# Optimization experiments

Measured on AMD Instinct MI355X. Metric: run time of the kernel, lower is better.

## Reference

```python
import jax, jax.numpy as jnp
import numpy as np

S, D, H, F = 4096, 1024, 16, 4096
DH = D // H  # 64
EPS = 1e-6


def _layer_norm(x, scale, bias):
    mu = jnp.mean(x, axis=-1, keepdims=True)
    var = jnp.mean(jnp.square(x - mu), axis=-1, keepdims=True)
    return (x - mu) * jax.lax.rsqrt(var + EPS) * scale + bias


def setup_inputs() -> dict:
    key = jax.random.key(0)
    ks = jax.random.split(key, 12)
    s = 0.02
    return {
        "x": jax.random.normal(ks[0], (S, D), jnp.float32),
        "Wq": jax.random.normal(ks[1], (D, H, DH), jnp.float32) * s,
        "bq": jnp.zeros((H, DH), jnp.float32),
        "Wk": jax.random.normal(ks[2], (D, H, DH), jnp.float32) * s,
        "bk": jnp.zeros((H, DH), jnp.float32),
        "Wv": jax.random.normal(ks[3], (D, H, DH), jnp.float32) * s,
        "bv": jnp.zeros((H, DH), jnp.float32),
        "Wo": jax.random.normal(ks[4], (H, DH, D), jnp.float32) * s,
        "bo": jnp.zeros((D,), jnp.float32),
        "ln1_scale": jnp.ones((D,), jnp.float32),
        "ln1_bias": jnp.zeros((D,), jnp.float32),
        "ln2_scale": jnp.ones((D,), jnp.float32),
        "ln2_bias": jnp.zeros((D,), jnp.float32),
        "W1": jax.random.normal(ks[5], (D, F), jnp.float32) * s,
        "b1": jnp.zeros((F,), jnp.float32),
        "W2": jax.random.normal(ks[6], (F, D), jnp.float32) * s,
        "b2": jnp.zeros((D,), jnp.float32),
    }


def reference(x, Wq, bq, Wk, bk, Wv, bv, Wo, bo,
              ln1_scale, ln1_bias, ln2_scale, ln2_bias,
              W1, b1, W2, b2):
    # --- attention block (pre-LN, no mask, no dropout, no RoPE) ---
    y = _layer_norm(x, ln1_scale, ln1_bias)            # [S, D]
    q = jnp.einsum("sd,dhk->shk", y, Wq) + bq          # [S, H, DH]
    k = jnp.einsum("sd,dhk->shk", y, Wk) + bk
    v = jnp.einsum("sd,dhk->shk", y, Wv) + bv
    scale = jnp.float32(1.0 / np.sqrt(DH))
    scores = jnp.einsum("qhd,khd->hqk", q * scale, k)  # [H, S, S]
    w = jax.nn.softmax(scores, axis=-1)
    ctx = jnp.einsum("hqk,khd->qhd", w, v)             # [S, H, DH]
    attn_out = jnp.einsum("qhd,hdo->qo", ctx, Wo) + bo  # [S, D]
    x = x + attn_out
    # --- FFN block ---
    y = _layer_norm(x, ln2_scale, ln2_bias)
    y = jax.nn.gelu(y @ W1 + b1, approximate=False)
    y = y @ W2 + b2
    return x + y
```

## Files before the change

kernel.cpp:

```cpp
#include <hip/hip_runtime.h>
#include <cstdint>
#include <cstddef>


typedef __attribute__((ext_vector_type(8))) __bf16 bf16x8;
typedef __attribute__((ext_vector_type(4))) float f32x4;
typedef __attribute__((ext_vector_type(2))) float f32x2;
typedef __attribute__((ext_vector_type(16))) float f32x16;
typedef __attribute__((ext_vector_type(4))) unsigned int u32x4;

__device__ inline unsigned short f2bf(float f) {
  unsigned int u = __float_as_uint(f);
  u += 0x7fffu + ((u >> 16) & 1u);
  return (unsigned short)(u >> 16);
}

__device__ inline void gload_lds16(const unsigned short* g, unsigned short* l) {
  __builtin_amdgcn_global_load_lds(
      (const __attribute__((address_space(1))) void*)g,
      (__attribute__((address_space(3))) void*)l, 16, 0, 0);
}

__global__ __launch_bounds__(256) void prep_all(
    const float* __restrict__ Wq, const float* __restrict__ Wk,
    const float* __restrict__ Wv, const float* __restrict__ Wo,
    const float* __restrict__ W1, const float* __restrict__ W2,
    const float* __restrict__ bq, const float* __restrict__ bk,
    const float* __restrict__ bv,
    unsigned short* __restrict__ WqkvT, unsigned short* __restrict__ WoT,
    unsigned short* __restrict__ W1T, unsigned short* __restrict__ W2T,
    float* __restrict__ bqkv) {
  int b = blockIdx.x;
  if (b < 12) {
    int i = b * 256 + threadIdx.x;
    bqkv[i] = (i < 1024) ? bq[i] : (i < 2048 ? bk[i - 1024] : bv[i - 2048]);
    return;
  }
  b -= 12;
  const float* in;
  unsigned short* out;
  int K, N, nbx;
  if (b < 4096) {
    const int sel = b >> 10;
    in = (sel == 0) ? Wq : (sel == 1) ? Wk : (sel == 2) ? Wv : Wo;
    out = (sel == 3) ? WoT : WqkvT + (size_t)sel * 1024 * 1024;
    K = 1024; N = 1024; nbx = 32; b &= 1023;
  } else if (b < 8192) {
    b -= 4096; in = W1; out = W1T; K = 1024; N = 4096; nbx = 128;
  } else {
    b -= 8192; in = W2; out = W2T; K = 4096; N = 1024; nbx = 32;
  }
  const int nb = (b % nbx) * 32, kb = (b / nbx) * 32;
  __shared__ float t[32][33];
  const int tx = threadIdx.x & 31, ty = threadIdx.x >> 5;
#pragma unroll
  for (int i = 0; i < 32; i += 8)
    t[ty + i][tx] = in[(size_t)(kb + ty + i) * N + nb + tx];
  __syncthreads();
#pragma unroll
  for (int i = 0; i < 32; i += 8)
    out[(size_t)(nb + ty + i) * K + kb + tx] = f2bf(t[tx][ty + i]);
}

__global__ __launch_bounds__(256) void ln_kernel(const float* __restrict__ x,
                                                 const float* __restrict__ gamma,
                                                 const float* __restrict__ beta,
                                                 unsigned short* __restrict__ y) {
  int row = blockIdx.x, tid = threadIdx.x;
  const float4 v = ((const float4*)(x + (size_t)row * 1024))[tid];
  float s = v.x + v.y + v.z + v.w;
#pragma unroll
  for (int off = 1; off < 64; off <<= 1) s += __shfl_xor(s, off);
  __shared__ float red1[4], red2[4];
  int wave = tid >> 6;
  if ((tid & 63) == 0) red1[wave] = s;
  __syncthreads();
  float mu = (red1[0] + red1[1] + red1[2] + red1[3]) * (1.0f / 1024.0f);
  float dx = v.x - mu, dy = v.y - mu, dz = v.z - mu, dw = v.w - mu;
  float s2 = dx * dx + dy * dy + dz * dz + dw * dw;
#pragma unroll
  for (int off = 1; off < 64; off <<= 1) s2 += __shfl_xor(s2, off);
  if ((tid & 63) == 0) red2[wave] = s2;
  __syncthreads();
  float var = (red2[0] + red2[1] + red2[2] + red2[3]) * (1.0f / 1024.0f);
  float inv = rsqrtf(var + 1e-6f);
  int c = tid * 4;
  ushort4 o;
  o.x = f2bf(dx * inv * gamma[c + 0] + beta[c + 0]);
  o.y = f2bf(dy * inv * gamma[c + 1] + beta[c + 1]);
  o.z = f2bf(dz * inv * gamma[c + 2] + beta[c + 2]);
  o.w = f2bf(dw * inv * gamma[c + 3] + beta[c + 3]);
  ((ushort4*)(y + (size_t)row * 1024))[tid] = o;
}

template <bool GELU, bool RES, bool OUTBF, bool SCALEQ>
__global__ __launch_bounds__(512, 2) void gemm8(
    const unsigned short* __restrict__ A,
    const unsigned short* __restrict__ BT,
    const float* __restrict__ bias,
    const float* __restrict__ res,
    void* __restrict__ out,
    int M, int N, int K) {
  constexpr int SLOT = 512 * 64;
  __shared__ unsigned short lds[2 * SLOT];
  (void)M;

  const int nbn = N / 256;
  const int bid = blockIdx.x;
  const int cpx = (int)gridDim.x >> 3;
  const int swzb = (bid & 7) * cpx + (bid >> 3);
  const int bm = swzb / nbn, bn = swzb % nbn;
  const int tid = threadIdx.x;
  const int lane = tid & 63, quad = lane >> 4, l16 = lane & 15;
  const int wm = tid >> 8, wn = (tid >> 6) & 3;

  const int rs = tid >> 3;
  const int xo = ((tid & 7) ^ (rs & 7)) * 8;
  const unsigned short* aSrc = A + (size_t)(bm * 256 + rs) * K + xo;
  const unsigned short* bSrc = BT + (size_t)(bn * 256 + rs) * K + xo;

  const int sw0 = (quad ^ (l16 & 7)) * 8;
  const int sw1 = ((quad ^ 4) ^ (l16 & 7)) * 8;
  const int aBase = (wm * 128 + l16) * 64;
  const int bBase = 16384 + (wn * 64 + l16) * 64;

  f32x4 acc[8][4];
  const f32x4 z4 = {0.f, 0.f, 0.f, 0.f};
#pragma unroll
  for (int i = 0; i < 8; ++i)
#pragma unroll
    for (int n = 0; n < 4; ++n) acc[i][n] = z4;

  const int NT = K >> 6;
  {
    unsigned short* dA = lds + (size_t)tid * 8;
    unsigned short* dB = lds + 16384 + (size_t)tid * 8;
#pragma unroll
    for (int u = 0; u < 4; ++u) gload_lds16(aSrc + (size_t)u * 64 * K, dA + u * 4096);
#pragma unroll
    for (int u = 0; u < 4; ++u) gload_lds16(bSrc + (size_t)u * 64 * K, dB + u * 4096);
  }

  for (int j = 0; j < NT; ++j) {
    const int s = j & 1;
    asm volatile("s_waitcnt vmcnt(0) lgkmcnt(0)" ::: "memory");
    __builtin_amdgcn_s_barrier();
    __builtin_amdgcn_sched_barrier(0);
    const unsigned short* Ts = lds + s * SLOT;
    unsigned short* stA = lds + (s ^ 1) * SLOT + (size_t)tid * 8;
    unsigned short* stB = stA + 16384;
    const bool pre = (j + 1 < NT);
    const int kN = (j + 1) << 6;

    bf16x8 af[4][2], bfr[4][2];
#pragma unroll
    for (int mm = 0; mm < 4; ++mm) {
      af[mm][0] = *(const bf16x8*)(Ts + aBase + mm * 1024 + sw0);
      af[mm][1] = *(const bf16x8*)(Ts + aBase + mm * 1024 + sw1);
    }
#pragma unroll
    for (int nn = 0; nn < 2; ++nn) {
      bfr[nn][0] = *(const bf16x8*)(Ts + bBase + nn * 1024 + sw0);
      bfr[nn][1] = *(const bf16x8*)(Ts + bBase + nn * 1024 + sw1);
    }
    if (pre) {
#pragma unroll
      for (int u = 0; u < 4; ++u)
        gload_lds16(aSrc + (size_t)u * 64 * K + kN, stA + u * 4096);
#pragma unroll
      for (int u = 0; u < 4; ++u)
        gload_lds16(bSrc + (size_t)u * 64 * K + kN, stB + u * 4096);
    }
    __builtin_amdgcn_s_barrier();
    __builtin_amdgcn_s_setprio(1);
#pragma unroll
    for (int mm = 0; mm < 4; ++mm)
#pragma unroll
      for (int nn = 0; nn < 2; ++nn) {
        acc[mm][nn] = __builtin_amdgcn_mfma_f32_16x16x32_bf16(af[mm][0], bfr[nn][0], acc[mm][nn], 0, 0, 0);
        acc[mm][nn] = __builtin_amdgcn_mfma_f32_16x16x32_bf16(af[mm][1], bfr[nn][1], acc[mm][nn], 0, 0, 0);
      }
    __builtin_amdgcn_s_setprio(0);
#pragma unroll
    for (int nn = 2; nn < 4; ++nn) {
      bfr[nn][0] = *(const bf16x8*)(Ts + bBase + nn * 1024 + sw0);
      bfr[nn][1] = *(const bf16x8*)(Ts + bBase + nn * 1024 + sw1);
    }
    __builtin_amdgcn_s_barrier();
    __builtin_amdgcn_s_setprio(1);
#pragma unroll
    for (int mm = 0; mm < 4; ++mm)
#pragma unroll
      for (int nn = 2; nn < 4; ++nn) {
        acc[mm][nn] = __builtin_amdgcn_mfma_f32_16x16x32_bf16(af[mm][0], bfr[nn][0], acc[mm][nn], 0, 0, 0);
        acc[mm][nn] = __builtin_amdgcn_mfma_f32_16x16x32_bf16(af[mm][1], bfr[nn][1], acc[mm][nn], 0, 0, 0);
      }
    __builtin_amdgcn_s_setprio(0);
#pragma unroll
    for (int mm = 0; mm < 4; ++mm) {
      af[mm][0] = *(const bf16x8*)(Ts + aBase + 4096 + mm * 1024 + sw0);
      af[mm][1] = *(const bf16x8*)(Ts + aBase + 4096 + mm * 1024 + sw1);
    }
    __builtin_amdgcn_s_barrier();
    __builtin_amdgcn_s_setprio(1);
#pragma unroll
    for (int mm = 0; mm < 4; ++mm)
#pragma unroll
      for (int nn = 0; nn < 2; ++nn) {
        acc[4 + mm][nn] = __builtin_amdgcn_mfma_f32_16x16x32_bf16(af[mm][0], bfr[nn][0], acc[4 + mm][nn], 0, 0, 0);
        acc[4 + mm][nn] = __builtin_amdgcn_mfma_f32_16x16x32_bf16(af[mm][1], bfr[nn][1], acc[4 + mm][nn], 0, 0, 0);
      }
    __builtin_amdgcn_s_setprio(0);
    __builtin_amdgcn_s_barrier();
    __builtin_amdgcn_s_setprio(1);
#pragma unroll
    for (int mm = 0; mm < 4; ++mm)
#pragma unroll
      for (int nn = 2; nn < 4; ++nn) {
        acc[4 + mm][nn] = __builtin_amdgcn_mfma_f32_16x16x32_bf16(af[mm][0], bfr[nn][0], acc[4 + mm][nn], 0, 0, 0);
        acc[4 + mm][nn] = __builtin_amdgcn_mfma_f32_16x16x32_bf16(af[mm][1], bfr[nn][1], acc[4 + mm][nn], 0, 0, 0);
      }
    __builtin_amdgcn_s_setprio(0);
  }

#pragma unroll
  for (int mi = 0; mi < 8; ++mi) {
    const int row0 = bm * 256 + wm * 128 + mi * 16 + quad * 4;
#pragma unroll
    for (int ni = 0; ni < 4; ++ni) {
      const int col = bn * 256 + wn * 64 + ni * 16 + l16;
      const float bv = bias[col];
      const float qs = (SCALEQ && col < 1024) ? 0.18033688f : 1.0f;
#pragma unroll
      for (int r = 0; r < 4; ++r) {
        float v = (acc[mi][ni][r] + bv) * qs;
        if (GELU) v = 0.5f * v * (1.0f + erff(v * 0.70710678118654752440f));
        if (RES) v += res[(size_t)(row0 + r) * N + col];
        if (OUTBF)
          ((unsigned short*)out)[(size_t)(row0 + r) * N + col] = f2bf(v);
        else
          ((float*)out)[(size_t)(row0 + r) * N + col] = v;
      }
    }
  }
}

template <bool GELU, bool RES, bool OUTBF>
__global__ __launch_bounds__(512, 2) void gemm3s(
    const unsigned short* __restrict__ A,
    const unsigned short* __restrict__ BT,
    const float* __restrict__ bias,
    const float* __restrict__ res,
    void* __restrict__ out,
    int M, int N, int K) {
  constexpr int SLOT = 256 * 64;
  __shared__ unsigned short lds[3 * SLOT];
  (void)M;

  const int nbn = N / 128;
  const int bid = blockIdx.x;
  const int cpx = (int)gridDim.x >> 3;
  const int swzb = (bid & 7) * cpx + (bid >> 3);
  const int bm = swzb / nbn, bn = swzb % nbn;
  const int tid = threadIdx.x;
  const int lane = tid & 63, quad = lane >> 4, l16 = lane & 15;
  const int wm = tid >> 8, wn = (tid >> 6) & 3;

  const int rs = tid >> 3;
  const int xo = ((tid & 7) ^ (rs & 7)) * 8;
  const unsigned short* aSrc = A + (size_t)(bm * 128 + rs) * K + xo;
  const unsigned short* bSrc = BT + (size_t)(bn * 128 + rs) * K + xo;

  const int sw0 = (quad ^ (l16 & 7)) * 8;
  const int sw1 = ((quad ^ 4) ^ (l16 & 7)) * 8;
  const int aBase = (wm * 64 + l16) * 64;
  const int bBase = 8192 + (wn * 32 + l16) * 64;

  f32x4 acc[4][2];
  const f32x4 z4 = {0.f, 0.f, 0.f, 0.f};
#pragma unroll
  for (int i = 0; i < 4; ++i)
#pragma unroll
    for (int n = 0; n < 2; ++n) acc[i][n] = z4;

  const int NT = K >> 6;
  {
    unsigned short* d0 = lds + (size_t)tid * 8;
    gload_lds16(aSrc, d0);
    gload_lds16(aSrc + (size_t)64 * K, d0 + 4096);
    gload_lds16(bSrc, d0 + 8192);
    gload_lds16(bSrc + (size_t)64 * K, d0 + 8192 + 4096);
    if (NT > 1) {
      unsigned short* d1 = lds + SLOT + (size_t)tid * 8;
      gload_lds16(aSrc + 64, d1);
      gload_lds16(aSrc + (size_t)64 * K + 64, d1 + 4096);
      gload_lds16(bSrc + 64, d1 + 8192);
      gload_lds16(bSrc + (size_t)64 * K + 64, d1 + 8192 + 4096);
    }
  }

  int sl = 0;
  for (int j = 0; j < NT; ++j) {
    if (j + 1 < NT)
      asm volatile("s_waitcnt vmcnt(4) lgkmcnt(0)" ::: "memory");
    else
      asm volatile("s_waitcnt vmcnt(0) lgkmcnt(0)" ::: "memory");
    __builtin_amdgcn_s_barrier();
    __builtin_amdgcn_sched_barrier(0);
    const unsigned short* Ts = lds + sl * SLOT;
    const int sl2 = (sl >= 1) ? sl - 1 : 2;
    unsigned short* st = lds + sl2 * SLOT + (size_t)tid * 8;

    bf16x8 af[2][2], bfr[2][2];
#pragma unroll
    for (int mm = 0; mm < 2; ++mm) {
      af[mm][0] = *(const bf16x8*)(Ts + aBase + mm * 1024 + sw0);
      af[mm][1] = *(const bf16x8*)(Ts + aBase + mm * 1024 + sw1);
    }
#pragma unroll
    for (int nn = 0; nn < 2; ++nn) {
      bfr[nn][0] = *(const bf16x8*)(Ts + bBase + nn * 1024 + sw0);
      bfr[nn][1] = *(const bf16x8*)(Ts + bBase + nn * 1024 + sw1);
    }
    if (j + 2 < NT) {
      const int kN = (j + 2) << 6;
      gload_lds16(aSrc + kN, st);
      gload_lds16(aSrc + (size_t)64 * K + kN, st + 4096);
      gload_lds16(bSrc + kN, st + 8192);
      gload_lds16(bSrc + (size_t)64 * K + kN, st + 8192 + 4096);
    }
    __builtin_amdgcn_s_barrier();
    __builtin_amdgcn_s_setprio(1);
#pragma unroll
    for (int mm = 0; mm < 2; ++mm)
#pragma unroll
      for (int nn = 0; nn < 2; ++nn) {
        acc[mm][nn] = __builtin_amdgcn_mfma_f32_16x16x32_bf16(af[mm][0], bfr[nn][0], acc[mm][nn], 0, 0, 0);
        acc[mm][nn] = __builtin_amdgcn_mfma_f32_16x16x32_bf16(af[mm][1], bfr[nn][1], acc[mm][nn], 0, 0, 0);
      }
    __builtin_amdgcn_s_setprio(0);
#pragma unroll
    for (int mm = 0; mm < 2; ++mm) {
      af[mm][0] = *(const bf16x8*)(Ts + aBase + 2048 + mm * 1024 + sw0);
      af[mm][1] = *(const bf16x8*)(Ts + aBase + 2048 + mm * 1024 + sw1);
    }
    __builtin_amdgcn_s_barrier();
    __builtin_amdgcn_s_setprio(1);
#pragma unroll
    for (int mm = 0; mm < 2; ++mm)
#pragma unroll
      for (int nn = 0; nn < 2; ++nn) {
        acc[2 + mm][nn] = __builtin_amdgcn_mfma_f32_16x16x32_bf16(af[mm][0], bfr[nn][0], acc[2 + mm][nn], 0, 0, 0);
        acc[2 + mm][nn] = __builtin_amdgcn_mfma_f32_16x16x32_bf16(af[mm][1], bfr[nn][1], acc[2 + mm][nn], 0, 0, 0);
      }
    __builtin_amdgcn_s_setprio(0);
    sl = (sl == 2) ? 0 : sl + 1;
  }

#pragma unroll
  for (int mi = 0; mi < 4; ++mi) {
    const int row0 = bm * 128 + wm * 64 + mi * 16 + quad * 4;
#pragma unroll
    for (int ni = 0; ni < 2; ++ni) {
      const int col = bn * 128 + wn * 32 + ni * 16 + l16;
      const float bv = bias[col];
#pragma unroll
      for (int r = 0; r < 4; ++r) {
        float v = acc[mi][ni][r] + bv;
        if (GELU) v = 0.5f * v * (1.0f + erff(v * 0.70710678118654752440f));
        if (RES) v += res[(size_t)(row0 + r) * N + col];
        if (OUTBF)
          ((unsigned short*)out)[(size_t)(row0 + r) * N + col] = f2bf(v);
        else
          ((float*)out)[(size_t)(row0 + r) * N + col] = v;
      }
    }
  }
}

__global__ __launch_bounds__(256) void prep_kv(const unsigned short* __restrict__ qkv,
                                               unsigned short* __restrict__ Kp,
                                               unsigned short* __restrict__ Vp) {
  __shared__ unsigned short Vt[64 * 64];
  int t = blockIdx.x, h = blockIdx.y;
  int tid = threadIdx.x;
  const int r2 = tid >> 3, c0 = (tid & 7) * 8;
  size_t tb = ((size_t)h * 64 + t) * 4096;
  {
    const unsigned short* kp = qkv + (size_t)(t * 64 + r2) * 3072 + 1024 + h * 64 + c0;
    uint4 k0 = *(const uint4*)kp;
    uint4 k1 = *(const uint4*)(kp + (size_t)32 * 3072);
    int c = c0 >> 3;
    *(uint4*)(Kp + tb + c * 512 + r2 * 8) = k0;
    *(uint4*)(Kp + tb + c * 512 + (r2 + 32) * 8) = k1;
  }
  {
    const unsigned short* vp = qkv + (size_t)(t * 64 + 2 * r2) * 3072 + 2048 + h * 64 + c0;
    uint4 v0 = *(const uint4*)vp;
    uint4 v1 = *(const uint4*)(vp + 3072);
    const unsigned short* p0 = (const unsigned short*)&v0;
    const unsigned short* p1 = (const unsigned short*)&v1;
#pragma unroll
    for (int dd = 0; dd < 8; dd++) {
      unsigned int pk = (unsigned int)p0[dd] | ((unsigned int)p1[dd] << 16);
      *(unsigned int*)&Vt[(c0 + dd) * 64 + 2 * r2] = pk;
    }
  }
  __syncthreads();
#pragma unroll
  for (int u0 = 0; u0 < 2; u0++) {
    int u = tid + u0 * 256;
    *(uint4*)(Vp + tb + u * 8) = *(const uint4*)&Vt[(u & 63) * 64 + (u >> 6) * 8];
  }
}

__global__ __launch_bounds__(256, 3) void attn_kernel(const unsigned short* __restrict__ qkv,
                                                      const unsigned short* __restrict__ Kp,
                                                      const unsigned short* __restrict__ Vp,
                                                      unsigned short* __restrict__ ctx) {
  __shared__ float comb[2 * 32 * 64];
  __shared__ float lpart[4 * 32];
  int qt = blockIdx.x, h = blockIdx.y;
  int tid = threadIdx.x;
  int w = tid >> 6, lane = tid & 63;
  int l31 = lane & 31, hi = lane >> 5;
  int qsub = w & 1, kvh = w >> 1;

  bf16x8 qf[4];
  {
    const unsigned short* qp = qkv + (size_t)(qt * 64 + qsub * 32 + l31) * 3072 + h * 64 + hi * 8;
#pragma unroll
    for (int kk = 0; kk < 4; kk++) qf[kk] = *(const bf16x8*)(qp + kk * 16);
  }

  const size_t hb = (size_t)h * 64 * 4096;
  const unsigned short* kB = Kp + hb + hi * 512 + (kvh * 32 + l31) * 8;
  const unsigned short* vB = Vp + hb + (kvh * 4 + hi) * 512 + l31 * 8;

  f32x16 accO0, accO1;
  f32x2 lp2 = {0.f, 0.f};
#pragma unroll
  for (int r = 0; r < 16; r++) { accO0[r] = 0.f; accO1[r] = 0.f; }

  bf16x8 kf[4];
#pragma unroll
  for (int kk = 0; kk < 4; kk++) kf[kk] = *(const bf16x8*)(kB + kk * 1024);

  for (int t = 0; t < 64; t++) {
    const unsigned short* vt = vB + (size_t)t * 4096;
    bf16x8 vA0 = *(const bf16x8*)(vt);
    bf16x8 vA1 = *(const bf16x8*)(vt + 1024);
    bf16x8 vB0 = *(const bf16x8*)(vt + 256);
    bf16x8 vB1 = *(const bf16x8*)(vt + 1024 + 256);

    f32x16 accS;
#pragma unroll
    for (int r = 0; r < 16; r++) accS[r] = 0.f;
#pragma unroll
    for (int kk = 0; kk < 4; kk++)
      accS = __builtin_amdgcn_mfma_f32_32x32x16_bf16(kf[kk], qf[kk], accS, 0, 0, 0);

    if (t < 63) {
      const unsigned short* kt = kB + (size_t)(t + 1) * 4096;
#pragma unroll
      for (int kk = 0; kk < 4; kk++) kf[kk] = *(const bf16x8*)(kt + kk * 1024);
    }

    unsigned int pd[8];
#pragma unroll
    for (int i = 0; i < 8; i++) {
      float a = __builtin_amdgcn_exp2f(accS[2 * i]);
      float b = __builtin_amdgcn_exp2f(accS[2 * i + 1]);
      f32x2 ab = {a, b};
      lp2 += ab;
      pd[i] = __builtin_amdgcn_perm(__float_as_uint(b), __float_as_uint(a), 0x07060302);
    }
    asm("v_permlane32_swap_b32 %0, %1" : "+v"(pd[0]), "+v"(pd[2]));
    asm("v_permlane32_swap_b32 %0, %1" : "+v"(pd[1]), "+v"(pd[3]));
    asm("v_permlane32_swap_b32 %0, %1" : "+v"(pd[4]), "+v"(pd[6]));
    asm("v_permlane32_swap_b32 %0, %1" : "+v"(pd[5]), "+v"(pd[7]));
    u32x4 f0 = {pd[0], pd[1], pd[2], pd[3]};
    u32x4 f1 = {pd[4], pd[5], pd[6], pd[7]};
    bf16x8 pa0 = __builtin_bit_cast(bf16x8, f0);
    bf16x8 pa1 = __builtin_bit_cast(bf16x8, f1);

    accO0 = __builtin_amdgcn_mfma_f32_32x32x16_bf16(pa0, vA0, accO0, 0, 0, 0);
    accO1 = __builtin_amdgcn_mfma_f32_32x32x16_bf16(pa0, vB0, accO1, 0, 0, 0);
    accO0 = __builtin_amdgcn_mfma_f32_32x32x16_bf16(pa1, vA1, accO0, 0, 0, 0);
    accO1 = __builtin_amdgcn_mfma_f32_32x32x16_bf16(pa1, vB1, accO1, 0, 0, 0);
  }

  float lp = lp2.x + lp2.y;
  lp += __shfl_xor(lp, 32);
  if (hi == 0) lpart[(kvh * 2 + qsub) * 32 + l31] = lp;
  if (kvh == 1) {
#pragma unroll
    for (int r = 0; r < 16; r++) {
      int q = (r & 3) + 8 * (r >> 2) + 4 * hi;
      comb[(qsub * 32 + q) * 64 + l31] = accO0[r];
      comb[(qsub * 32 + q) * 64 + 32 + l31] = accO1[r];
    }
  }
  __syncthreads();
  if (kvh == 0) {
#pragma unroll
    for (int r = 0; r < 16; r++) {
      int q = (r & 3) + 8 * (r >> 2) + 4 * hi;
      float l = lpart[qsub * 32 + q] + lpart[(2 + qsub) * 32 + q];
      float inv = 1.0f / l;
      float v0 = (accO0[r] + comb[(qsub * 32 + q) * 64 + l31]) * inv;
      float v1 = (accO1[r] + comb[(qsub * 32 + q) * 64 + 32 + l31]) * inv;
      int row = qt * 64 + qsub * 32 + q;
      size_t o = (size_t)row * 1024 + h * 64;
      ctx[o + l31] = f2bf(v0);
      ctx[o + 32 + l31] = f2bf(v1);
    }
  }
}

extern "C" void kernel_launch(void* const* d_in, const int* in_sizes, int n_in,
                              void* d_out, int out_size, void* d_ws, size_t ws_size,
                              hipStream_t stream) {
  const float* x   = (const float*)d_in[0];
  const float* Wq  = (const float*)d_in[1];
  const float* bq  = (const float*)d_in[2];
  const float* Wk  = (const float*)d_in[3];
  const float* bk  = (const float*)d_in[4];
  const float* Wv  = (const float*)d_in[5];
  const float* bv  = (const float*)d_in[6];
  const float* Wo  = (const float*)d_in[7];
  const float* bo  = (const float*)d_in[8];
  const float* g1  = (const float*)d_in[9];
  const float* be1 = (const float*)d_in[10];
  const float* g2  = (const float*)d_in[11];
  const float* be2 = (const float*)d_in[12];
  const float* W1  = (const float*)d_in[13];
  const float* b1  = (const float*)d_in[14];
  const float* W2  = (const float*)d_in[15];
  const float* b2  = (const float*)d_in[16];
  float* out = (float*)d_out;

  char* p = (char*)d_ws;
  unsigned short* WqkvT = (unsigned short*)p; p += (size_t)3072 * 1024 * 2;
  unsigned short* WoT   = (unsigned short*)p; p += (size_t)1024 * 1024 * 2;
  unsigned short* W1T   = (unsigned short*)p; p += (size_t)4096 * 1024 * 2;
  unsigned short* W2T   = (unsigned short*)p; p += (size_t)1024 * 4096 * 2;
  float*          bqkv  = (float*)p;          p += 16384;
  unsigned short* y1    = (unsigned short*)p; p += (size_t)4096 * 1024 * 2;
  unsigned short* qkvb  = (unsigned short*)p; p += (size_t)4096 * 3072 * 2;
  unsigned short* ctxb  = (unsigned short*)p; p += (size_t)4096 * 1024 * 2;
  float*          x1    = (float*)p;          p += (size_t)4096 * 1024 * 4;
  unsigned short* Kp    = (unsigned short*)p; p += (size_t)16 * 64 * 4096 * 2;
  unsigned short* Vp    = (unsigned short*)p; p += (size_t)16 * 64 * 4096 * 2;
  unsigned short* hbuf  = qkvb;

  dim3 b256(256);
  dim3 b512(512);
  prep_all<<<dim3(12300), b256, 0, stream>>>(Wq, Wk, Wv, Wo, W1, W2, bq, bk, bv,
                                             WqkvT, WoT, W1T, W2T, bqkv);

  ln_kernel<<<4096, b256, 0, stream>>>(x, g1, be1, y1);
  gemm8<false, false, true, true><<<dim3(192), b512, 0, stream>>>(y1, WqkvT, bqkv, nullptr, qkvb, 4096, 3072, 1024);
  prep_kv<<<dim3(64, 16), b256, 0, stream>>>(qkvb, Kp, Vp);
  attn_kernel<<<dim3(64, 16), b256, 0, stream>>>(qkvb, Kp, Vp, ctxb);
  gemm3s<false, true, false><<<dim3(256), b512, 0, stream>>>(ctxb, WoT, bo, x, x1, 4096, 1024, 1024);
  ln_kernel<<<4096, b256, 0, stream>>>(x1, g2, be2, y1);
  gemm8<true, false, true, false><<<dim3(256), b512, 0, stream>>>(y1, W1T, b1, nullptr, hbuf, 4096, 4096, 1024);
  gemm3s<false, true, false><<<dim3(256), b512, 0, stream>>>(hbuf, W2T, b2, x1, out, 4096, 1024, 4096);
}
```

Measured before the change: 367.5 us.

## Fuse first layernorm into prep kernel and drop KV split in attention

The first LayerNorm is folded into the weight-prep launch as extra blocks, removing one kernel launch. The attention kernel no longer splits the KV range across wave pairs with an LDS combine. Each wave now owns 32 distinct queries (128 per block) and walks all 4096 keys in 128 half-tiles, so the grid shrinks to 32x16 blocks. This removes the cross-wave reduction and LDS traffic, but leaves fewer blocks and longer serial loops per wave, which could hurt occupancy on 256 CUs.

```diff
diff --git a/kernel.cpp b/kernel.cpp
--- a/kernel.cpp
+++ b/kernel.cpp
@@ -27,16 +27,48 @@
     const float* __restrict__ W1, const float* __restrict__ W2,
     const float* __restrict__ bq, const float* __restrict__ bk,
     const float* __restrict__ bv,
+    const float* __restrict__ x, const float* __restrict__ g1,
+    const float* __restrict__ be1, unsigned short* __restrict__ y1,
     unsigned short* __restrict__ WqkvT, unsigned short* __restrict__ WoT,
     unsigned short* __restrict__ W1T, unsigned short* __restrict__ W2T,
     float* __restrict__ bqkv) {
   int b = blockIdx.x;
+  const int tid = threadIdx.x;
   if (b < 12) {
-    int i = b * 256 + threadIdx.x;
+    int i = b * 256 + tid;
     bqkv[i] = (i < 1024) ? bq[i] : (i < 2048 ? bk[i - 1024] : bv[i - 2048]);
     return;
   }
   b -= 12;
+  if (b < 4096) {
+    const int row = b;
+    const float4 v = ((const float4*)(x + (size_t)row * 1024))[tid];
+    float s = v.x + v.y + v.z + v.w;
+#pragma unroll
+    for (int off = 1; off < 64; off <<= 1) s += __shfl_xor(s, off);
+    __shared__ float red1[4], red2[4];
+    int wave = tid >> 6;
+    if ((tid & 63) == 0) red1[wave] = s;
+    __syncthreads();
+    float mu = (red1[0] + red1[1] + red1[2] + red1[3]) * (1.0f / 1024.0f);
+    float dx = v.x - mu, dy = v.y - mu, dz = v.z - mu, dw = v.w - mu;
+    float s2 = dx * dx + dy * dy + dz * dz + dw * dw;
+#pragma unroll
+    for (int off = 1; off < 64; off <<= 1) s2 += __shfl_xor(s2, off);
+    if ((tid & 63) == 0) red2[wave] = s2;
+    __syncthreads();
+    float var = (red2[0] + red2[1] + red2[2] + red2[3]) * (1.0f / 1024.0f);
+    float inv = rsqrtf(var + 1e-6f);
+    int c = tid * 4;
+    ushort4 o;
+    o.x = f2bf(dx * inv * g1[c + 0] + be1[c + 0]);
+    o.y = f2bf(dy * inv * g1[c + 1] + be1[c + 1]);
+    o.z = f2bf(dz * inv * g1[c + 2] + be1[c + 2]);
+    o.w = f2bf(dw * inv * g1[c + 3] + be1[c + 3]);
+    ((ushort4*)(y1 + (size_t)row * 1024))[tid] = o;
+    return;
+  }
+  b -= 4096;
   const float* in;
   unsigned short* out;
   int K, N, nbx;
@@ -52,7 +84,7 @@
   }
   const int nb = (b % nbx) * 32, kb = (b / nbx) * 32;
   __shared__ float t[32][33];
-  const int tx = threadIdx.x & 31, ty = threadIdx.x >> 5;
+  const int tx = tid & 31, ty = tid >> 5;
 #pragma unroll
   for (int i = 0; i < 32; i += 8)
     t[ty + i][tx] = in[(size_t)(kb + ty + i) * N + nb + tx];
@@ -418,24 +450,22 @@
                                                       const unsigned short* __restrict__ Kp,
                                                       const unsigned short* __restrict__ Vp,
                                                       unsigned short* __restrict__ ctx) {
-  __shared__ float comb[2 * 32 * 64];
-  __shared__ float lpart[4 * 32];
+  __shared__ float lpw[4 * 32];
   int qt = blockIdx.x, h = blockIdx.y;
   int tid = threadIdx.x;
   int w = tid >> 6, lane = tid & 63;
   int l31 = lane & 31, hi = lane >> 5;
-  int qsub = w & 1, kvh = w >> 1;
 
   bf16x8 qf[4];
   {
-    const unsigned short* qp = qkv + (size_t)(qt * 64 + qsub * 32 + l31) * 3072 + h * 64 + hi * 8;
+    const unsigned short* qp = qkv + (size_t)(qt * 128 + w * 32 + l31) * 3072 + h * 64 + hi * 8;
 #pragma unroll
     for (int kk = 0; kk < 4; kk++) qf[kk] = *(const bf16x8*)(qp + kk * 16);
   }
 
   const size_t hb = (size_t)h * 64 * 4096;
-  const unsigned short* kB = Kp + hb + hi * 512 + (kvh * 32 + l31) * 8;
-  const unsigned short* vB = Vp + hb + (kvh * 4 + hi) * 512 + l31 * 8;
+  const unsigned short* kB = Kp + hb + hi * 512 + l31 * 8;
+  const unsigned short* vB = Vp + hb + hi * 512 + l31 * 8;
 
   f32x16 accO0, accO1;
   f32x2 lp2 = {0.f, 0.f};
@@ -446,8 +476,8 @@
 #pragma unroll
   for (int kk = 0; kk < 4; kk++) kf[kk] = *(const bf16x8*)(kB + kk * 1024);
 
-  for (int t = 0; t < 64; t++) {
-    const unsigned short* vt = vB + (size_t)t * 4096;
+  for (int u = 0; u < 128; u++) {
+    const unsigned short* vt = vB + (size_t)(u >> 1) * 4096 + (u & 1) * 2048;
     bf16x8 vA0 = *(const bf16x8*)(vt);
     bf16x8 vA1 = *(const bf16x8*)(vt + 1024);
     bf16x8 vB0 = *(const bf16x8*)(vt + 256);
@@ -460,8 +490,9 @@
     for (int kk = 0; kk < 4; kk++)
       accS = __builtin_amdgcn_mfma_f32_32x32x16_bf16(kf[kk], qf[kk], accS, 0, 0, 0);
 
-    if (t < 63) {
-      const unsigned short* kt = kB + (size_t)(t + 1) * 4096;
+    if (u < 127) {
+      const int un = u + 1;
+      const unsigned short* kt = kB + (size_t)(un >> 1) * 4096 + (un & 1) * 256;
 #pragma unroll
       for (int kk = 0; kk < 4; kk++) kf[kk] = *(const bf16x8*)(kt + kk * 1024);
     }
@@ -492,29 +523,16 @@
 
   float lp = lp2.x + lp2.y;
   lp += __shfl_xor(lp, 32);
-  if (hi == 0) lpart[(kvh * 2 + qsub) * 32 + l31] = lp;
-  if (kvh == 1) {
-#pragma unroll
-    for (int r = 0; r < 16; r++) {
-      int q = (r & 3) + 8 * (r >> 2) + 4 * hi;
-      comb[(qsub * 32 + q) * 64 + l31] = accO0[r];
-      comb[(qsub * 32 + q) * 64 + 32 + l31] = accO1[r];
-    }
-  }
+  if (hi == 0) lpw[w * 32 + l31] = lp;
   __syncthreads();
-  if (kvh == 0) {
-#pragma unroll
-    for (int r = 0; r < 16; r++) {
-      int q = (r & 3) + 8 * (r >> 2) + 4 * hi;
-      float l = lpart[qsub * 32 + q] + lpart[(2 + qsub) * 32 + q];
-      float inv = 1.0f / l;
-      float v0 = (accO0[r] + comb[(qsub * 32 + q) * 64 + l31]) * inv;
-      float v1 = (accO1[r] + comb[(qsub * 32 + q) * 64 + 32 + l31]) * inv;
-      int row = qt * 64 + qsub * 32 + q;
-      size_t o = (size_t)row * 1024 + h * 64;
-      ctx[o + l31] = f2bf(v0);
-      ctx[o + 32 + l31] = f2bf(v1);
-    }
+#pragma unroll
+  for (int r = 0; r < 16; r++) {
+    int q = (r & 3) + 8 * (r >> 2) + 4 * hi;
+    float inv = 1.0f / lpw[w * 32 + q];
+    int row = qt * 128 + w * 32 + q;
+    size_t o = (size_t)row * 1024 + h * 64;
+    ctx[o + l31] = f2bf(accO0[r] * inv);
+    ctx[o + 32 + l31] = f2bf(accO1[r] * inv);
   }
 }
 
@@ -556,13 +574,13 @@
 
   dim3 b256(256);
   dim3 b512(512);
-  prep_all<<<dim3(12300), b256, 0, stream>>>(Wq, Wk, Wv, Wo, W1, W2, bq, bk, bv,
+  prep_all<<<dim3(16396), b256, 0, stream>>>(Wq, Wk, Wv, Wo, W1, W2, bq, bk, bv,
+                                             x, g1, be1, y1,
                                              WqkvT, WoT, W1T, W2T, bqkv);
 
-  ln_kernel<<<4096, b256, 0, stream>>>(x, g1, be1, y1);
   gemm8<false, false, true, true><<<dim3(192), b512, 0, stream>>>(y1, WqkvT, bqkv, nullptr, qkvb, 4096, 3072, 1024);
   prep_kv<<<dim3(64, 16), b256, 0, stream>>>(qkvb, Kp, Vp);
-  attn_kernel<<<dim3(64, 16), b256, 0, stream>>>(qkvb, Kp, Vp, ctxb);
+  attn_kernel<<<dim3(32, 16), b256, 0, stream>>>(qkvb, Kp, Vp, ctxb);
   gemm3s<false, true, false><<<dim3(256), b512, 0, stream>>>(ctxb, WoT, bo, x, x1, 4096, 1024, 1024);
   ln_kernel<<<4096, b256, 0, stream>>>(x1, g2, be2, y1);
   gemm8<true, false, true, false><<<dim3(256), b512, 0, stream>>>(y1, W1T, b1, nullptr, hbuf, 4096, 4096, 1024);
```

Measured after the change: 391.1 us. 1.06x slower.
